# Optimization experiments

Hardware: AMD Instinct MI355X
Metric: run time of the kernel (lower is better)

Reference implementation:

```python
import jax, jax.numpy as jnp
import numpy as np

N_NODES = 100000
IN_CH = 128
HID = 128   # 2 * out_channels
OUT = 64    # out_channels
N_EDGES = 1000000


def _glorot(key, shape):
    lim = np.sqrt(6.0 / (shape[0] + shape[1]))
    return jax.random.uniform(key, shape, jnp.float32, -lim, lim)


def setup_inputs() -> dict:
    key = jax.random.key(0)
    ks = jax.random.split(key, 8)
    x = jax.random.normal(ks[0], (N_NODES, IN_CH), jnp.float32)
    edge_index = jax.random.randint(ks[1], (2, N_EDGES), 0, N_NODES, jnp.int64)
    return {
        "x": x,
        "edge_index": edge_index,
        # conv1: in -> 2*out
        "W1_l": _glorot(ks[2], (IN_CH, HID)),
        "W1_r": _glorot(ks[3], (IN_CH, HID)),
        "b1": jnp.zeros((HID,), jnp.float32),
        # conv_mu: 2*out -> out
        "Wmu_l": _glorot(ks[4], (HID, OUT)),
        "Wmu_r": _glorot(ks[5], (HID, OUT)),
        "bmu": jnp.zeros((OUT,), jnp.float32),
        # conv_logstd: 2*out -> out
        "Wls_l": _glorot(ks[6], (HID, OUT)),
        "Wls_r": _glorot(ks[7], (HID, OUT)),
        "bls": jnp.zeros((OUT,), jnp.float32),
    }


def _sage_conv(x, src, dst, W_l, W_r, b, n_nodes):
    # mean-aggregate neighbor features: messages flow src -> dst (PyG source_to_target)
    agg = jax.ops.segment_sum(x[src], dst, num_segments=n_nodes)          # [N, d]
    deg = jax.ops.segment_sum(jnp.ones(src.shape, x.dtype), dst, num_segments=n_nodes)
    agg = agg / jnp.maximum(deg, 1.0)[:, None]
    return agg @ W_l + x @ W_r + b


def reference(x, edge_index, W1_l, W1_r, b1, Wmu_l, Wmu_r, bmu, Wls_l, Wls_r, bls):
    src, dst = edge_index[0], edge_index[1]
    n = x.shape[0]
    h = jax.nn.relu(_sage_conv(x, src, dst, W1_l, W1_r, b1, n))
    mu = _sage_conv(h, src, dst, Wmu_l, Wmu_r, bmu, n)
    logstd = _sage_conv(h, src, dst, Wls_l, Wls_r, bls, n)
    return (mu, logstd)
```

## Files before the change

kernel.cpp:

```cpp
#include <hip/hip_runtime.h>

#define NN 100000
#define IC 128
#define OC 64
#define NE 1000000

#define NBUCK 256
#define BN 392
#define RCAP 4608
#define EPB 2048
#define CAPA 24
#define GPAD 16
#define LDW 136
#define BINA_GRID 489
#define CVT_BLOCKS 6250

typedef __attribute__((ext_vector_type(8))) short short8;
typedef __attribute__((ext_vector_type(4))) float f32x4;

static __device__ __forceinline__ float b2f(unsigned short u) {
    unsigned v = ((unsigned)u) << 16;
    float f;
    __builtin_memcpy(&f, &v, 4);
    return f;
}
static __device__ __forceinline__ unsigned short f2b(float f) {
    unsigned u;
    __builtin_memcpy(&u, &f, 4);
    u += 0x7fff + ((u >> 16) & 1);
    return (unsigned short)(u >> 16);
}

#if defined(__has_builtin)
#if __has_builtin(__builtin_amdgcn_cvt_pk_fp8_f32) && __has_builtin(__builtin_amdgcn_cvt_pk_f32_fp8)
#define HW_FP8 1
#endif
#endif

static __device__ __forceinline__ unsigned f2q1(float f) {
    unsigned u;
    __builtin_memcpy(&u, &f, 4);
    unsigned s = (u >> 24) & 0x80u;
    unsigned a = u & 0x7FFFFFFFu;
    if (a < 0x3C000000u) return s;
    if (a < 0x3C800000u) return s | 0x08u;
    if (a >= 0x43E00000u) return s | 0x7Eu;
    a += 0x7FFFFu + ((a >> 20) & 1u);
    unsigned e = (a >> 23) - 120u;
    unsigned m = (a >> 20) & 7u;
    unsigned c = (e << 3) | m;
    if (c > 0x7Eu) c = 0x7Eu;
    return s | c;
}
static __device__ __forceinline__ float q1f(unsigned q) {
    unsigned em = q & 0x7Fu;
    unsigned s = (q & 0x80u) << 24;
    unsigned u = (em >= 8u) ? (s | (((em >> 3) + 120u) << 23) | ((em & 7u) << 20)) : s;
    float f;
    __builtin_memcpy(&f, &u, 4);
    return f;
}

static __device__ __forceinline__ unsigned pack4_fp8(float a, float b, float c, float d) {
#ifdef HW_FP8
    int r = __builtin_amdgcn_cvt_pk_fp8_f32(a, b, 0, false);
    r = __builtin_amdgcn_cvt_pk_fp8_f32(c, d, r, true);
    return (unsigned)r;
#else
    return f2q1(a) | (f2q1(b) << 8) | (f2q1(c) << 16) | (f2q1(d) << 24);
#endif
}

__device__ __forceinline__ void binA_body(int blk, int t,
                                          const int* __restrict__ src,
                                          const int* __restrict__ dst,
                                          int* __restrict__ gcur,
                                          unsigned* __restrict__ bins,
                                          unsigned (*buf)[CAPA], int* lcnt, int* goff) {
    lcnt[t] = 0;
    __syncthreads();
    const int e0 = blk * EPB;
#pragma unroll
    for (int q = 0; q < EPB / 256; ++q) {
        int e = e0 + q * 256 + t;
        if (e < NE) {
            int d = dst[e];
            int s = src[e];
            int b = d / BN;
            unsigned packed = ((unsigned)(d - b * BN) << 17) | (unsigned)s;
            int idx = atomicAdd(&lcnt[b], 1);
            if (idx < CAPA) {
                buf[b][idx] = packed;
            } else {
                int g = atomicAdd(&gcur[b * GPAD], 1);
                if (g < RCAP) bins[(size_t)b * RCAP + g] = packed;
            }
        }
    }
    __syncthreads();
    int c = lcnt[t];
    if (c > CAPA) c = CAPA;
    if (c > 0) goff[t] = atomicAdd(&gcur[t * GPAD], c);
    __syncthreads();
    const int wid = t >> 6, lane = t & 63;
    for (int b = wid * 64; b < wid * 64 + 64; ++b) {
        int cb = lcnt[b];
        if (cb > CAPA) cb = CAPA;
        if (lane < cb) {
            int g = goff[b] + lane;
            if (g < RCAP) bins[(size_t)b * RCAP + g] = buf[b][lane];
        }
    }
}

__global__ __launch_bounds__(256) void k_front(
    const int* __restrict__ src, const int* __restrict__ dst,
    int* __restrict__ gcur, unsigned* __restrict__ bins,
    const float* __restrict__ x, unsigned short* __restrict__ xb,
    unsigned char* __restrict__ xq,
    const float* __restrict__ W1l, const float* __restrict__ W1r,
    const float* __restrict__ Wml, const float* __restrict__ Wmr,
    const float* __restrict__ Wsl, const float* __restrict__ Wsr,
    unsigned short* __restrict__ Wf1, unsigned short* __restrict__ Wf2) {
    __shared__ unsigned buf[NBUCK][CAPA];
    __shared__ int lcnt[NBUCK];
    __shared__ int goff[NBUCK];
    const int blk = blockIdx.x;
    const int tid = threadIdx.x;
    if (blk < BINA_GRID) {
        binA_body(blk, tid, src, dst, gcur, bins, buf, lcnt, goff);
    } else if (blk < BINA_GRID + CVT_BLOCKS) {
        int t = (blk - BINA_GRID) * 256 + tid;
        const float4* p = (const float4*)x + (size_t)t * 2;
        float4 f0 = p[0], f1 = p[1];
        short8 o;
        o[0] = (short)f2b(f0.x); o[1] = (short)f2b(f0.y);
        o[2] = (short)f2b(f0.z); o[3] = (short)f2b(f0.w);
        o[4] = (short)f2b(f1.x); o[5] = (short)f2b(f1.y);
        o[6] = (short)f2b(f1.z); o[7] = (short)f2b(f1.w);
        *((short8*)xb + t) = o;
        uint2 q;
        q.x = pack4_fp8(f0.x, f0.y, f0.z, f0.w);
        q.y = pack4_fp8(f1.x, f1.y, f1.z, f1.w);
        *((uint2*)xq + t) = q;
    } else {
        int t = (blk - BINA_GRID - CVT_BLOCKS) * 256 + tid;
        if (t >= 2 * 4096) return;
        const int layer = t >> 12;
        const int f = t & 4095;
        const int lane = f & 63;
        const int nt = (f >> 6) & 7;
        const int ks = f >> 9;
        const int col = nt * 16 + (lane & 15);
        const int kb = ks * 32 + ((lane >> 4) << 3);
        short8 o;
#pragma unroll
        for (int e = 0; e < 8; ++e) {
            const int k = kb + e;
            float v;
            if (layer == 0) {
                v = (k < 128) ? W1l[k * 128 + col] : W1r[(k - 128) * 128 + col];
            } else {
                if (col < OC) v = (k < 128) ? Wml[k * OC + col] : Wmr[(k - 128) * OC + col];
                else {
                    int c2 = col - OC;
                    v = (k < 128) ? Wsl[k * OC + c2] : Wsr[(k - 128) * OC + c2];
                }
            }
            o[e] = (short)f2b(v);
        }
        unsigned short* W = (layer == 0) ? Wf1 : Wf2;
        *(short8*)(W + (size_t)f * 8) = o;
    }
}

__global__ __launch_bounds__(256) void k_binB(const int* __restrict__ gcur,
                                              const unsigned* __restrict__ bins,
                                              int* __restrict__ row_ptr,
                                              int* __restrict__ csr) {
    __shared__ int lc[512];
    __shared__ int rk[512];
    __shared__ int tsum[256];
    __shared__ int seg[RCAP];
    __shared__ int sh_bs;
    const int b = blockIdx.x;
    const int t = threadIdx.x;
    const int base = b * BN;
    const int nloc = (NN - base < BN) ? (NN - base) : BN;
    int v = gcur[t * GPAD];
    if (v > RCAP) v = RCAP;
    tsum[t] = v;
    __syncthreads();
    for (int off = 1; off < 256; off <<= 1) {
        int u = (t >= off) ? tsum[t - off] : 0;
        __syncthreads();
        tsum[t] += u;
        __syncthreads();
    }
    if (t == b) sh_bs = tsum[t] - v;
    if (b == 0 && t == 255) row_ptr[NN] = tsum[255];
    lc[t] = 0; lc[t + 256] = 0;
    rk[t] = 0; rk[t + 256] = 0;
    __syncthreads();
    int c = gcur[b * GPAD];
    if (c > RCAP) c = RCAP;
    const unsigned* mb = bins + (size_t)b * RCAP;
    for (int i = t; i < c; i += 256) atomicAdd(&lc[mb[i] >> 17], 1);
    __syncthreads();
    int l0 = lc[2 * t], l1 = lc[2 * t + 1];
    int s = l0 + l1;
    tsum[t] = s;
    __syncthreads();
    for (int off = 1; off < 256; off <<= 1) {
        int u = (t >= off) ? tsum[t - off] : 0;
        __syncthreads();
        tsum[t] += u;
        __syncthreads();
    }
    int run = tsum[t] - s;
    lc[2 * t] = run;
    lc[2 * t + 1] = run + l0;
    __syncthreads();
    const int bs = sh_bs;
    for (int i = t; i < nloc; i += 256) row_ptr[base + i] = bs + lc[i];
    for (int i = t; i < c; i += 256) {
        unsigned p = mb[i];
        int dl = p >> 17;
        int r = atomicAdd(&rk[dl], 1);
        seg[lc[dl] + r] = (int)(p & 0x1FFFFu);
    }
    __syncthreads();
    for (int i = t; i < c; i += 256) csr[bs + i] = seg[i];
}

template <int FP8>
__global__ __launch_bounds__(256) void k_agg(const unsigned short* __restrict__ feat,
                                             const unsigned char* __restrict__ featq,
                                             const int* __restrict__ row_ptr,
                                             const int* __restrict__ csr,
                                             unsigned short* __restrict__ agg) {
    const int lane = threadIdx.x & 63;
    const int wid = threadIdx.x >> 6;
    const int slot = lane >> 4;
    const int cg = lane & 15;
    const int node = blockIdx.x * 16 + wid * 4 + slot;
    if (node >= NN) return;
    const int beg = row_ptr[node];
    const int end = row_ptr[node + 1];
    float acc[8];
#pragma unroll
    for (int q = 0; q < 8; ++q) acc[q] = 0.f;

    if (FP8) {
        for (int j = beg; j < end; j += 8) {
            const int nl = end - j;
            uint2 v[8];
#pragma unroll
            for (int u = 0; u < 8; ++u) {
                if (u < nl) {
                    int s = csr[j + u];
                    v[u] = *(const uint2*)(featq + (size_t)s * IC + cg * 8);
                }
            }
#pragma unroll
            for (int u = 0; u < 8; ++u) {
                if (u < nl) {
#ifdef HW_FP8
                    auto p0 = __builtin_amdgcn_cvt_pk_f32_fp8((int)v[u].x, false);
                    auto p1 = __builtin_amdgcn_cvt_pk_f32_fp8((int)v[u].x, true);
                    auto p2 = __builtin_amdgcn_cvt_pk_f32_fp8((int)v[u].y, false);
                    auto p3 = __builtin_amdgcn_cvt_pk_f32_fp8((int)v[u].y, true);
                    acc[0] += p0[0]; acc[1] += p0[1];
                    acc[2] += p1[0]; acc[3] += p1[1];
                    acc[4] += p2[0]; acc[5] += p2[1];
                    acc[6] += p3[0]; acc[7] += p3[1];
#else
#pragma unroll
                    for (int q = 0; q < 4; ++q) acc[q] += q1f((v[u].x >> (8 * q)) & 0xFFu);
#pragma unroll
                    for (int q = 0; q < 4; ++q) acc[4 + q] += q1f((v[u].y >> (8 * q)) & 0xFFu);
#endif
                }
            }
        }
    } else {
        for (int j = beg; j < end; j += 8) {
            const int nl = end - j;
            short8 v[8];
#pragma unroll
            for (int u = 0; u < 8; ++u) {
                if (u < nl) {
                    int s = csr[j + u];
                    v[u] = *(const short8*)(feat + (size_t)s * IC + cg * 8);
                }
            }
#pragma unroll
            for (int u = 0; u < 8; ++u) {
                if (u < nl) {
#pragma unroll
                    for (int q = 0; q < 8; ++q) acc[q] += b2f((unsigned short)v[u][q]);
                }
            }
        }
    }
    float inv = 1.0f / fmaxf((float)(end - beg), 1.0f);
    short8 o;
#pragma unroll
    for (int q = 0; q < 8; ++q) o[q] = (short)f2b(acc[q] * inv);
    *(short8*)(agg + (size_t)node * IC + cg * 8) = o;
}

template <int MODE>
__global__ __launch_bounds__(256) void k_gemm(
    const unsigned short* __restrict__ Agg, const unsigned short* __restrict__ Xb,
    const unsigned short* __restrict__ Wf,
    const float* __restrict__ bias0, const float* __restrict__ bias1,
    unsigned short* __restrict__ hout, float* __restrict__ out_mu,
    float* __restrict__ out_ls) {
    const int lane = threadIdx.x & 63;
    const int wid = threadIdx.x >> 6;
    const int rowg = blockIdx.x * 128 + wid * 32;
    const int r16 = lane & 15;
    const int k8 = (lane >> 4) * 8;

    __shared__ unsigned short smem[MODE == 0 ? (4 * 32 * LDW) : 16384];
    short8* bsm = (short8*)smem;

    int rA[2];
#pragma unroll
    for (int m = 0; m < 2; ++m) {
        int r = rowg + m * 16 + r16;
        rA[m] = (r < NN) ? r : (NN - 1);
    }

    short8 aF[2][8];
#pragma unroll
    for (int ks = 0; ks < 4; ++ks) {
        aF[0][ks] = *(const short8*)(Agg + (size_t)rA[0] * IC + ks * 32 + k8);
        aF[1][ks] = *(const short8*)(Agg + (size_t)rA[1] * IC + ks * 32 + k8);
    }
#pragma unroll
    for (int ks = 0; ks < 4; ++ks) {
        aF[0][4 + ks] = *(const short8*)(Xb + (size_t)rA[0] * IC + ks * 32 + k8);
        aF[1][4 + ks] = *(const short8*)(Xb + (size_t)rA[1] * IC + ks * 32 + k8);
    }

    const short8* Wg = (const short8*)Wf;
#pragma unroll
    for (int i = 0; i < 8; ++i)
        bsm[i * 256 + threadIdx.x] = Wg[i * 256 + threadIdx.x];

#pragma unroll
    for (int ks = 0; ks < 8; ++ks)
        asm volatile("" :: "v"(aF[0][ks]), "v"(aF[1][ks]));

    __syncthreads();

    f32x4 acc[2][8];
#pragma unroll
    for (int m = 0; m < 2; ++m)
#pragma unroll
        for (int nt = 0; nt < 8; ++nt) acc[m][nt] = (f32x4){0.f, 0.f, 0.f, 0.f};

#pragma unroll
    for (int ks = 0; ks < 4; ++ks) {
        short8 bF[8];
#pragma unroll
        for (int nt = 0; nt < 8; ++nt) bF[nt] = bsm[(ks * 8 + nt) * 64 + lane];
#pragma unroll
        for (int nt = 0; nt < 8; ++nt) {
            acc[0][nt] = __builtin_amdgcn_mfma_f32_16x16x32_bf16(aF[0][ks], bF[nt], acc[0][nt], 0, 0, 0);
            acc[1][nt] = __builtin_amdgcn_mfma_f32_16x16x32_bf16(aF[1][ks], bF[nt], acc[1][nt], 0, 0, 0);
        }
    }
    __syncthreads();
#pragma unroll
    for (int i = 0; i < 8; ++i)
        bsm[i * 256 + threadIdx.x] = Wg[2048 + i * 256 + threadIdx.x];
    __syncthreads();
#pragma unroll
    for (int ks = 4; ks < 8; ++ks) {
        short8 bF[8];
#pragma unroll
        for (int nt = 0; nt < 8; ++nt) bF[nt] = bsm[((ks - 4) * 8 + nt) * 64 + lane];
#pragma unroll
        for (int nt = 0; nt < 8; ++nt) {
            acc[0][nt] = __builtin_amdgcn_mfma_f32_16x16x32_bf16(aF[0][ks], bF[nt], acc[0][nt], 0, 0, 0);
            acc[1][nt] = __builtin_amdgcn_mfma_f32_16x16x32_bf16(aF[1][ks], bF[nt], acc[1][nt], 0, 0, 0);
        }
    }

    const int rbase = (lane >> 4) * 4;
    if (MODE == 0) {
        __syncthreads();
        unsigned short* ws = smem + wid * 32 * LDW;
#pragma unroll
        for (int m = 0; m < 2; ++m) {
#pragma unroll
            for (int nt = 0; nt < 8; ++nt) {
                const int c = nt * 16 + r16;
                const float bv = bias0[c];
#pragma unroll
                for (int q = 0; q < 4; ++q) {
                    float v = fmaxf(acc[m][nt][q] + bv, 0.f);
                    ws[(m * 16 + rbase + q) * LDW + c] = f2b(v);
                }
            }
        }
        __syncthreads();
#pragma unroll
        for (int p = 0; p < 8; ++p) {
            const int rloc = p * 4 + (lane >> 4);
            const int row = rowg + rloc;
            if (row < NN) {
                short8 v = *(const short8*)&ws[rloc * LDW + r16 * 8];
                *(short8*)(hout + (size_t)row * IC + r16 * 8) = v;
            }
        }
    } else {
#pragma unroll
        for (int m = 0; m < 2; ++m) {
#pragma unroll
            for (int nt = 0; nt < 8; ++nt) {
                const int c = nt * 16 + r16;
                const float bv = (c < OC) ? bias0[c] : bias1[c - OC];
#pragma unroll
                for (int q = 0; q < 4; ++q) {
                    const int row = rowg + m * 16 + rbase + q;
                    if (row >= NN) continue;
                    float v = acc[m][nt][q] + bv;
                    if (c < OC) out_mu[(size_t)row * OC + c] = v;
                    else        out_ls[(size_t)row * OC + (c - OC)] = v;
                }
            }
        }
    }
}

extern "C" void kernel_launch(void* const* d_in, const int* in_sizes, int n_in,
                              void* d_out, int out_size, void* d_ws, size_t ws_size,
                              hipStream_t stream) {
    const float* x   = (const float*)d_in[0];
    const int*   ei  = (const int*)d_in[1];
    const float* W1l = (const float*)d_in[2];
    const float* W1r = (const float*)d_in[3];
    const float* b1  = (const float*)d_in[4];
    const float* Wml = (const float*)d_in[5];
    const float* Wmr = (const float*)d_in[6];
    const float* bm  = (const float*)d_in[7];
    const float* Wsl = (const float*)d_in[8];
    const float* Wsr = (const float*)d_in[9];
    const float* bs  = (const float*)d_in[10];

    const int* src = ei;
    const int* dst = ei + NE;

    char* w = (char*)d_ws;
    unsigned short* xb   = (unsigned short*)(w);
    unsigned short* hb   = (unsigned short*)(w + 25600000);
    unsigned short* aggb = (unsigned short*)(w + 51200000);
    unsigned short* Wf1  = (unsigned short*)(w + 76800000);
    unsigned short* Wf2  = (unsigned short*)(w + 76865536);
    int* row_ptr  = (int*)(w + 76931072);
    int* csr      = (int*)(w + 77331200);
    int* gcur     = (int*)(w + 81331200);
    unsigned* bins = (unsigned*)(w + 81347584);
    unsigned char* xq = (unsigned char*)(w + 86066176);

    float* out_mu = (float*)d_out;
    float* out_ls = out_mu + (size_t)NN * OC;

    const int gemm_grid = (NN + 127) / 128;
    const int agg_grid = (NN + 15) / 16;

    hipMemsetAsync(gcur, 0, NBUCK * GPAD * sizeof(int), stream);
    k_front<<<BINA_GRID + CVT_BLOCKS + 32, 256, 0, stream>>>(
        src, dst, gcur, bins, x, xb, xq, W1l, W1r, Wml, Wmr, Wsl, Wsr, Wf1, Wf2);
    k_binB<<<NBUCK, 256, 0, stream>>>(gcur, bins, row_ptr, csr);

    k_agg<1><<<agg_grid, 256, 0, stream>>>(nullptr, xq, row_ptr, csr, aggb);
    k_gemm<0><<<gemm_grid, 256, 0, stream>>>(aggb, xb, Wf1, b1, nullptr,
                                             hb, nullptr, nullptr);

    k_agg<0><<<agg_grid, 256, 0, stream>>>(hb, nullptr, row_ptr, csr, aggb);
    k_gemm<1><<<gemm_grid, 256, 0, stream>>>(aggb, hb, Wf2, bm, bs,
                                             nullptr, out_mu, out_ls);
}
```

Measured before the change: 174.1 us.

## Degree-sort nodes per bucket and widen FP8 aggregation loads to 16 bytes

During CSR construction, k_binB now builds a per-bucket counting sort of destination nodes by in-degree and writes an order array. Both aggregation kernels process nodes in that order, so nodes with similar degree share a wavefront and fewer lanes sit idle on divergent loop lengths. The FP8 aggregation also switches to 8 lanes per node with 16-byte loads, handling 32 nodes per block instead of 16. The cost is an extra indirection per node, scattered output writes, and some extra shared-memory atomics in binB.

Result: faster. 170.3 us (-2.2%).

```diff
diff --git a/kernel.cpp b/kernel.cpp
--- a/kernel.cpp
+++ b/kernel.cpp
@@ -68,6 +68,16 @@
     return (unsigned)r;
 #else
     return f2q1(a) | (f2q1(b) << 8) | (f2q1(c) << 16) | (f2q1(d) << 24);
+#endif
+}
+static __device__ __forceinline__ void dec4(unsigned w, float* o) {
+#ifdef HW_FP8
+    auto p0 = __builtin_amdgcn_cvt_pk_f32_fp8((int)w, false);
+    auto p1 = __builtin_amdgcn_cvt_pk_f32_fp8((int)w, true);
+    o[0] = p0[0]; o[1] = p0[1]; o[2] = p1[0]; o[3] = p1[1];
+#else
+#pragma unroll
+    for (int q = 0; q < 4; ++q) o[q] = q1f((w >> (8 * q)) & 0xFFu);
 #endif
 }
 
@@ -177,10 +187,12 @@
 __global__ __launch_bounds__(256) void k_binB(const int* __restrict__ gcur,
                                               const unsigned* __restrict__ bins,
                                               int* __restrict__ row_ptr,
-                                              int* __restrict__ csr) {
+                                              int* __restrict__ csr,
+                                              int* __restrict__ order) {
     __shared__ int lc[512];
     __shared__ int rk[512];
     __shared__ int tsum[256];
+    __shared__ int dh[64];
     __shared__ int seg[RCAP];
     __shared__ int sh_bs;
     const int b = blockIdx.x;
@@ -201,6 +213,7 @@
     if (b == 0 && t == 255) row_ptr[NN] = tsum[255];
     lc[t] = 0; lc[t + 256] = 0;
     rk[t] = 0; rk[t + 256] = 0;
+    if (t < 64) dh[t] = 0;
     __syncthreads();
     int c = gcur[b * GPAD];
     if (c > RCAP) c = RCAP;
@@ -208,6 +221,10 @@
     for (int i = t; i < c; i += 256) atomicAdd(&lc[mb[i] >> 17], 1);
     __syncthreads();
     int l0 = lc[2 * t], l1 = lc[2 * t + 1];
+    const int d0 = (l0 < 64) ? l0 : 63;
+    const int d1 = (l1 < 64) ? l1 : 63;
+    if (2 * t < nloc) atomicAdd(&dh[d0], 1);
+    if (2 * t + 1 < nloc) atomicAdd(&dh[d1], 1);
     int s = l0 + l1;
     tsum[t] = s;
     __syncthreads();
@@ -220,7 +237,18 @@
     int run = tsum[t] - s;
     lc[2 * t] = run;
     lc[2 * t + 1] = run + l0;
-    __syncthreads();
+    if (t < 64) {
+        int dv = dh[t];
+        int sc = dv;
+        for (int off = 1; off < 64; off <<= 1) {
+            int u = __shfl_up(sc, off, 64);
+            if (t >= off) sc += u;
+        }
+        dh[t] = sc - dv;
+    }
+    __syncthreads();
+    if (2 * t < nloc) { int p = atomicAdd(&dh[d0], 1); order[base + p] = base + 2 * t; }
+    if (2 * t + 1 < nloc) { int p = atomicAdd(&dh[d1], 1); order[base + p] = base + 2 * t + 1; }
     const int bs = sh_bs;
     for (int i = t; i < nloc; i += 256) row_ptr[base + i] = bs + lc[i];
     for (int i = t; i < c; i += 256) {
@@ -238,52 +266,61 @@
                                              const unsigned char* __restrict__ featq,
                                              const int* __restrict__ row_ptr,
                                              const int* __restrict__ csr,
+                                             const int* __restrict__ order,
                                              unsigned short* __restrict__ agg) {
     const int lane = threadIdx.x & 63;
     const int wid = threadIdx.x >> 6;
-    const int slot = lane >> 4;
-    const int cg = lane & 15;
-    const int node = blockIdx.x * 16 + wid * 4 + slot;
-    if (node >= NN) return;
-    const int beg = row_ptr[node];
-    const int end = row_ptr[node + 1];
-    float acc[8];
-#pragma unroll
-    for (int q = 0; q < 8; ++q) acc[q] = 0.f;
-
     if (FP8) {
+        const int slot = lane >> 3;
+        const int cl = lane & 7;
+        const int idx = blockIdx.x * 32 + wid * 8 + slot;
+        if (idx >= NN) return;
+        const int node = order[idx];
+        const int beg = row_ptr[node];
+        const int end = row_ptr[node + 1];
+        float acc[16];
+#pragma unroll
+        for (int q = 0; q < 16; ++q) acc[q] = 0.f;
         for (int j = beg; j < end; j += 8) {
             const int nl = end - j;
-            uint2 v[8];
+            uint4 v[8];
 #pragma unroll
             for (int u = 0; u < 8; ++u) {
                 if (u < nl) {
                     int s = csr[j + u];
-                    v[u] = *(const uint2*)(featq + (size_t)s * IC + cg * 8);
+                    v[u] = *(const uint4*)(featq + (size_t)s * IC + cl * 16);
                 }
             }
 #pragma unroll
             for (int u = 0; u < 8; ++u) {
                 if (u < nl) {
-#ifdef HW_FP8
-                    auto p0 = __builtin_amdgcn_cvt_pk_f32_fp8((int)v[u].x, false);
-                    auto p1 = __builtin_amdgcn_cvt_pk_f32_fp8((int)v[u].x, true);
-                    auto p2 = __builtin_amdgcn_cvt_pk_f32_fp8((int)v[u].y, false);
-                    auto p3 = __builtin_amdgcn_cvt_pk_f32_fp8((int)v[u].y, true);
-                    acc[0] += p0[0]; acc[1] += p0[1];
-                    acc[2] += p1[0]; acc[3] += p1[1];
-                    acc[4] += p2[0]; acc[5] += p2[1];
-                    acc[6] += p3[0]; acc[7] += p3[1];
-#else
-#pragma unroll
-                    for (int q = 0; q < 4; ++q) acc[q] += q1f((v[u].x >> (8 * q)) & 0xFFu);
-#pragma unroll
-                    for (int q = 0; q < 4; ++q) acc[4 + q] += q1f((v[u].y >> (8 * q)) & 0xFFu);
-#endif
-                }
-            }
-        }
+                    float d[16];
+                    dec4(v[u].x, d); dec4(v[u].y, d + 4);
+                    dec4(v[u].z, d + 8); dec4(v[u].w, d + 12);
+#pragma unroll
+                    for (int q = 0; q < 16; ++q) acc[q] += d[q];
+                }
+            }
+        }
+        float inv = 1.0f / fmaxf((float)(end - beg), 1.0f);
+        short8 o0, o1;
+#pragma unroll
+        for (int q = 0; q < 8; ++q) o0[q] = (short)f2b(acc[q] * inv);
+#pragma unroll
+        for (int q = 0; q < 8; ++q) o1[q] = (short)f2b(acc[8 + q] * inv);
+        *(short8*)(agg + (size_t)node * IC + cl * 16) = o0;
+        *(short8*)(agg + (size_t)node * IC + cl * 16 + 8) = o1;
     } else {
+        const int slot = lane >> 4;
+        const int cg = lane & 15;
+        const int idx = blockIdx.x * 16 + wid * 4 + slot;
+        if (idx >= NN) return;
+        const int node = order[idx];
+        const int beg = row_ptr[node];
+        const int end = row_ptr[node + 1];
+        float acc[8];
+#pragma unroll
+        for (int q = 0; q < 8; ++q) acc[q] = 0.f;
         for (int j = beg; j < end; j += 8) {
             const int nl = end - j;
             short8 v[8];
@@ -302,12 +339,12 @@
                 }
             }
         }
-    }
-    float inv = 1.0f / fmaxf((float)(end - beg), 1.0f);
-    short8 o;
-#pragma unroll
-    for (int q = 0; q < 8; ++q) o[q] = (short)f2b(acc[q] * inv);
-    *(short8*)(agg + (size_t)node * IC + cg * 8) = o;
+        float inv = 1.0f / fmaxf((float)(end - beg), 1.0f);
+        short8 o;
+#pragma unroll
+        for (int q = 0; q < 8; ++q) o[q] = (short)f2b(acc[q] * inv);
+        *(short8*)(agg + (size_t)node * IC + cg * 8) = o;
+    }
 }
 
 template <int MODE>
@@ -466,23 +503,25 @@
     int* gcur     = (int*)(w + 81331200);
     unsigned* bins = (unsigned*)(w + 81347584);
     unsigned char* xq = (unsigned char*)(w + 86066176);
+    int* order    = (int*)(w + 98866176);
 
     float* out_mu = (float*)d_out;
     float* out_ls = out_mu + (size_t)NN * OC;
 
     const int gemm_grid = (NN + 127) / 128;
-    const int agg_grid = (NN + 15) / 16;
+    const int agg1_grid = (NN + 31) / 32;
+    const int agg2_grid = (NN + 15) / 16;
 
     hipMemsetAsync(gcur, 0, NBUCK * GPAD * sizeof(int), stream);
     k_front<<<BINA_GRID + CVT_BLOCKS + 32, 256, 0, stream>>>(
         src, dst, gcur, bins, x, xb, xq, W1l, W1r, Wml, Wmr, Wsl, Wsr, Wf1, Wf2);
-    k_binB<<<NBUCK, 256, 0, stream>>>(gcur, bins, row_ptr, csr);
-
-    k_agg<1><<<agg_grid, 256, 0, stream>>>(nullptr, xq, row_ptr, csr, aggb);
+    k_binB<<<NBUCK, 256, 0, stream>>>(gcur, bins, row_ptr, csr, order);
+
+    k_agg<1><<<agg1_grid, 256, 0, stream>>>(nullptr, xq, row_ptr, csr, order, aggb);
     k_gemm<0><<<gemm_grid, 256, 0, stream>>>(aggb, xb, Wf1, b1, nullptr,
                                              hb, nullptr, nullptr);
 
-    k_agg<0><<<agg_grid, 256, 0, stream>>>(hb, nullptr, row_ptr, csr, aggb);
+    k_agg<0><<<agg2_grid, 256, 0, stream>>>(hb, nullptr, row_ptr, csr, order, aggb);
     k_gemm<1><<<gemm_grid, 256, 0, stream>>>(aggb, hb, Wf2, bm, bs,
                                              nullptr, out_mu, out_ls);
 }
```
